# Performance work log

Hardware: AMD Instinct MI355X
Metric: run time of the kernel (lower is better)

The kernel has to match this reference:

```python
import jax, jax.numpy as jnp
import numpy as np

N, E, B = 100000, 1600000, 1024
EPS = 1e-5


def setup_inputs() -> dict:
    key = jax.random.key(0)
    ks = jax.random.split(key, 32)
    w = lambda k, shape: (jax.random.normal(k, shape, jnp.float32) * 0.05)
    inp = {
        'x': jax.random.normal(ks[0], (N, 20), jnp.float32),
        'edge_index': jax.random.randint(ks[1], (2, E), 0, N, dtype=jnp.int32),
        'batch': jnp.sort(jax.random.randint(ks[2], (N,), 0, B, dtype=jnp.int32)),
        # GCN layer 1 (20->64) + BN
        'W1': w(ks[3], (20, 64)), 'b1': jnp.zeros(64), 'g1': jnp.ones(64), 'bt1': jnp.zeros(64),
        # GCN layer 2 (64->64) + BN
        'W2': w(ks[4], (64, 64)), 'b2': jnp.zeros(64), 'g2': jnp.ones(64), 'bt2': jnp.zeros(64),
        # GCN layer 3 (64->128)
        'W3': w(ks[5], (64, 128)), 'b3': jnp.zeros(128),
        # operation head
        'Wo1': w(ks[6], (128, 64)), 'bo1': jnp.zeros(64), 'Wo2': w(ks[7], (64, 13)), 'bo2': jnp.zeros(13),
        # param head
        'Wp1': w(ks[8], (128, 64)), 'bp1': jnp.zeros(64), 'Wp2': w(ks[9], (64, 64)), 'bp2': jnp.zeros(64), 'Wp3': w(ks[10], (64, 1)), 'bp3': jnp.zeros(1),
        # done head
        'Wd1': w(ks[11], (128, 64)), 'bd1': jnp.zeros(64), 'Wd2': w(ks[12], (64, 2)), 'bd2': jnp.zeros(2),
    }
    return inp


def _gcn(x, W, b, src, dst):
    # PyG GCNConv: sym-normalized A+I, linear first, bias after aggregation
    h = x @ W  # [N, F]
    deg = jax.ops.segment_sum(jnp.ones_like(src, jnp.float32), dst, N) + 1.0  # +1 self loop
    dinv = jax.lax.rsqrt(deg)
    norm = dinv[src] * dinv[dst]  # [E]
    agg = jax.ops.segment_sum(h[src] * norm[:, None], dst, N)
    agg = agg + h * (dinv * dinv)[:, None]  # self-loop term
    return agg + b


def _bn(x, g, bt):
    mu = jnp.mean(x, axis=0)
    var = jnp.mean((x - mu) ** 2, axis=0)  # biased var (torch BN training math)
    return (x - mu) * jax.lax.rsqrt(var + EPS) * g + bt


def reference(x, edge_index, batch, W1, b1, g1, bt1, W2, b2, g2, bt2, W3, b3,
              Wo1, bo1, Wo2, bo2, Wp1, bp1, Wp2, bp2, Wp3, bp3, Wd1, bd1, Wd2, bd2):
    src, dst = edge_index[0], edge_index[1]
    h = jax.nn.relu(_bn(_gcn(x, W1, b1, src, dst), g1, bt1))  # dropout = identity (eval)
    h = jax.nn.relu(_bn(_gcn(h, W2, b2, src, dst), g2, bt2))
    h = _gcn(h, W3, b3, src, dst)  # [N, 128]
    # global mean pool over graphs
    sums = jax.ops.segment_sum(h, batch, B)
    cnt = jax.ops.segment_sum(jnp.ones((N,), jnp.float32), batch, B)
    enc = sums / jnp.maximum(cnt, 1.0)[:, None]  # [B, 128]
    op_logits = jax.nn.relu(enc @ Wo1 + bo1) @ Wo2 + bo2  # [B, 13]
    p = jax.nn.relu(enc @ Wp1 + bp1)
    p = jax.nn.relu(p @ Wp2 + bp2)
    param_value = p @ Wp3 + bp3  # [B, 1]
    done_logits = jax.nn.relu(enc @ Wd1 + bd1) @ Wd2 + bd2  # [B, 2]
    return op_logits, param_value, done_logits, enc
```

## Files before the change

kernel.cpp:

```cpp
#include <hip/hip_runtime.h>

#define BN_EPS 1e-5f

constexpr int BSH = 9;
constexpr int MAXB = 200;
constexpr int CAP = 12288;
constexpr int BINCAP = 32;
constexpr int FLUSH = 16;
constexpr int SBLK = 256;


__global__ void initk(int* __restrict__ gcur, float* __restrict__ bn, int NB) {
  int t = blockIdx.x * blockDim.x + threadIdx.x;
  if (t < NB) gcur[t] = t * CAP;
  if (t < 512) bn[t] = 0.f;
}

__global__ void bound_kernel(const int* __restrict__ batch, int* __restrict__ goffs, int N, int B) {
  int i = blockIdx.x * blockDim.x + threadIdx.x;
  if (i < N) {
    int b = batch[i];
    int p = (i == 0) ? -1 : batch[i - 1];
    for (int g = p + 1; g <= b; ++g) goffs[g] = i;
    if (i == N - 1) {
      for (int g = b + 1; g <= B; ++g) goffs[g] = N;
    }
  }
}


__global__ __launch_bounds__(256) void passA(const int* __restrict__ dst, const int* __restrict__ src,
                                             int* __restrict__ gcur, unsigned long long* __restrict__ temp,
                                             int E, int NB) {
  __shared__ unsigned long long bins[MAXB * BINCAP];
  __shared__ int bcnt[MAXB];
  int tid = threadIdx.x;
  for (int b = tid; b < NB; b += 256) bcnt[b] = 0;
  __syncthreads();
  int chunk = (E + gridDim.x - 1) / gridDim.x;
  int e0 = blockIdx.x * chunk;
  int e1 = min(e0 + chunk, E);
  for (int base = e0; base < e1; base += 1024) {
#pragma unroll
    for (int j = 0; j < 4; ++j) {
      int e = base + tid * 4 + j;
      if (e < e1) {
        int d = dst[e];
        int s = src[e];
        int b = d >> BSH;
        unsigned long long pk = ((unsigned long long)(unsigned)s << 32) | (unsigned)d;
        int slot = atomicAdd(&bcnt[b], 1);
        if (slot < BINCAP) {
          bins[b * BINCAP + slot] = pk;
        } else {
          int p = atomicAdd(&gcur[b], 1);
          temp[p] = pk;
        }
      }
    }
    __syncthreads();
    if (tid < NB) {
      int c = min(bcnt[tid], BINCAP);
      while (c >= FLUSH) {
        int p = atomicAdd(&gcur[tid], FLUSH);
        for (int j = 0; j < FLUSH; ++j) temp[p + j] = bins[tid * BINCAP + j];
        c -= FLUSH;
        for (int j = 0; j < c; ++j) bins[tid * BINCAP + j] = bins[tid * BINCAP + FLUSH + j];
      }
      bcnt[tid] = c;
    }
    __syncthreads();
  }
  if (tid < NB) {
    int c = min(bcnt[tid], BINCAP);
    if (c > 0) {
      int p = atomicAdd(&gcur[tid], c);
      for (int j = 0; j < c; ++j) temp[p + j] = bins[tid * BINCAP + j];
    }
  }
}

__global__ __launch_bounds__(512) void passB1(const unsigned long long* __restrict__ temp,
                                              const int* __restrict__ gcur,
                                              int* __restrict__ deg, float* __restrict__ dinv, int N) {
  __shared__ int h[512];
  int b = blockIdx.x, t = threadIdx.x;
  h[t] = 0;
  __syncthreads();
  int cnt = min(gcur[b] - b * CAP, CAP);
  const unsigned long long* tp = temp + (size_t)b * CAP;
  for (int i = t; i < cnt; i += 512) {
    int d = (int)(tp[i] & 0xffffffffu);
    atomicAdd(&h[d & 511], 1);
  }
  __syncthreads();
  int node = (b << BSH) + t;
  if (node < N) {
    deg[node] = h[t];
    dinv[node] = rsqrtf((float)h[t] + 1.f);
  }
}

__global__ __launch_bounds__(512) void passB2(const unsigned long long* __restrict__ temp,
                                              const int* __restrict__ gcur,
                                              const int* __restrict__ offs,
                                              int* __restrict__ csr, int N) {
  __shared__ int lofs[512];
  __shared__ int lcnt[512];
  int b = blockIdx.x, t = threadIdx.x;
  int node = (b << BSH) + t;
  lofs[t] = offs[min(node, N)];
  lcnt[t] = 0;
  __syncthreads();
  int cnt = min(gcur[b] - b * CAP, CAP);
  const unsigned long long* tp = temp + (size_t)b * CAP;
  for (int i = t; i < cnt; i += 512) {
    unsigned long long pk = tp[i];
    int d = (int)(pk & 0xffffffffu) & 511;
    int s = (int)(pk >> 32);
    int pos = lofs[d] + atomicAdd(&lcnt[d], 1);
    csr[pos] = s;
  }
}


__global__ __launch_bounds__(1024) void scan_p1(const int* __restrict__ cnt,
                                                int* __restrict__ offs,
                                                int* __restrict__ bsum, int n) {
  __shared__ int sh[1024];
  int t = threadIdx.x;
  int i = blockIdx.x * 1024 + t;
  int v = (i < n) ? cnt[i] : 0;
  sh[t] = v;
  __syncthreads();
  for (int d = 1; d < 1024; d <<= 1) {
    int x = (t >= d) ? sh[t - d] : 0;
    __syncthreads();
    sh[t] += x;
    __syncthreads();
  }
  if (i < n) offs[i] = sh[t] - v;
  if (t == 1023) bsum[blockIdx.x] = sh[t];
}

__global__ void scan_p2(int* __restrict__ bsum, int nb) {
  __shared__ int sh[128];
  int t = threadIdx.x;
  int v = (t < nb) ? bsum[t] : 0;
  sh[t] = v;
  __syncthreads();
  for (int d = 1; d < 128; d <<= 1) {
    int x = (t >= d) ? sh[t - d] : 0;
    __syncthreads();
    sh[t] += x;
    __syncthreads();
  }
  if (t < nb) bsum[t] = sh[t] - v;
}

__global__ __launch_bounds__(1024) void scan_p3(int* __restrict__ offs,
                                                const int* __restrict__ bsum, int n, int E) {
  int i = blockIdx.x * 1024 + threadIdx.x;
  if (i < n) offs[i] += bsum[blockIdx.x];
  if (i == 0) offs[n] = E;
}


__global__ __launch_bounds__(256) void agg32x_kernel(const float* __restrict__ x,
                                                     const int* __restrict__ offs,
                                                     const int* __restrict__ csr,
                                                     const float* __restrict__ dinv,
                                                     float* __restrict__ out, int n) {
  int lane = threadIdx.x & 63;
  int wid = threadIdx.x >> 6;
  int half = lane >> 5, f = lane & 31;
  bool act = f < 20;
  int gw = blockIdx.x * 4 + wid, nw = gridDim.x * 4;
  for (int i = gw; i < n; i += nw) {
    float acc = 0.f;
    if (!half && act) acc = x[(size_t)i * 20 + f] * dinv[i];
    int st = offs[i], en = offs[i + 1];
    for (int base = st; base < en; base += 64) {
      int idx = base + lane;
      int v = (idx < en) ? csr[idx] : 0;
      int cnt = min(64, en - base);
      int j = 0;
      for (; j + 3 < cnt; j += 4) {
        int s0 = __shfl(v, j + half);
        int s1 = __shfl(v, j + 2 + half);
        if (act) acc += x[(size_t)s0 * 20 + f] * dinv[s0] + x[(size_t)s1 * 20 + f] * dinv[s1];
      }
      for (; j < cnt; ++j) {
        int s = __shfl(v, j);
        if (!half && act) acc += x[(size_t)s * 20 + f] * dinv[s];
      }
    }
    acc += __shfl_xor(acc, 32);
    if (!half) out[(size_t)i * 32 + f] = acc;
  }
}

template <bool SCALE>
__global__ __launch_bounds__(256) void agg64t_kernel(const float* __restrict__ z,
                                                     const float* __restrict__ tav,
                                                     const float* __restrict__ tcv,
                                                     const int* __restrict__ offs,
                                                     const int* __restrict__ csr,
                                                     const float* __restrict__ dinv,
                                                     float* __restrict__ out, int n) {
  int lane = threadIdx.x & 63;
  int wid = threadIdx.x >> 6;
  float ta = tav[lane], tc = tcv[lane];
  int gw = blockIdx.x * 4 + wid, nw = gridDim.x * 4;
  for (int i = gw; i < n; i += nw) {
    float di = dinv[i];
    float acc = fmaxf(z[(size_t)i * 64 + lane] * ta + tc, 0.f) * di;
    int st = offs[i], en = offs[i + 1];
    for (int base = st; base < en; base += 64) {
      int idx = base + lane;
      int v = (idx < en) ? csr[idx] : 0;
      int cnt = min(64, en - base);
      int j = 0;
      for (; j + 3 < cnt; j += 4) {
        int s0 = __shfl(v, j), s1 = __shfl(v, j + 1);
        int s2 = __shfl(v, j + 2), s3 = __shfl(v, j + 3);
        float d0 = dinv[s0], d1 = dinv[s1], d2 = dinv[s2], d3 = dinv[s3];
        acc += fmaxf(z[(size_t)s0 * 64 + lane] * ta + tc, 0.f) * d0 +
               fmaxf(z[(size_t)s1 * 64 + lane] * ta + tc, 0.f) * d1 +
               fmaxf(z[(size_t)s2 * 64 + lane] * ta + tc, 0.f) * d2 +
               fmaxf(z[(size_t)s3 * 64 + lane] * ta + tc, 0.f) * d3;
      }
      for (; j < cnt; ++j) {
        int s = __shfl(v, j);
        acc += fmaxf(z[(size_t)s * 64 + lane] * ta + tc, 0.f) * dinv[s];
      }
    }
    if (SCALE) acc *= di;
    out[(size_t)i * 64 + lane] = acc;
  }
}


template <int K, int AS>
__global__ __launch_bounds__(256) void gemm_agg(const float* __restrict__ A, const float* __restrict__ W,
                                                const float* __restrict__ bias, const float* __restrict__ dinv,
                                                float* __restrict__ z, int n) {
  __shared__ float Ws[K * 64];
  __shared__ float As[128 * (K + 1)];
  int tid = threadIdx.x;
  int row0 = blockIdx.x * 128;
  for (int i = tid; i < K * 64; i += 256) Ws[i] = W[i];
  for (int i = tid; i < 128 * K; i += 256) {
    int r = i / K, k = i - r * K;
    int gr = row0 + r;
    As[r * (K + 1) + k] = (gr < n) ? A[(size_t)gr * AS + k] : 0.f;
  }
  __syncthreads();
  int rg = tid >> 2;
  int fs = tid & 3;
  float acc0[16], acc1[16];
#pragma unroll
  for (int j = 0; j < 16; ++j) { acc0[j] = 0.f; acc1[j] = 0.f; }
  const float* a0 = &As[(2 * rg) * (K + 1)];
  const float* a1 = &As[(2 * rg + 1) * (K + 1)];
  const float* wb = &Ws[fs * 16];
  for (int k = 0; k < K; ++k) {
    float x0 = a0[k], x1 = a1[k];
#pragma unroll
    for (int j = 0; j < 16; ++j) {
      float w = wb[k * 64 + j];
      acc0[j] += x0 * w;
      acc1[j] += x1 * w;
    }
  }
  int r0 = row0 + 2 * rg;
  if (r0 < n) {
    float dv = dinv[r0];
    float4* zp = (float4*)&z[(size_t)r0 * 64 + fs * 16];
#pragma unroll
    for (int j = 0; j < 16; j += 4)
      zp[j >> 2] = make_float4(acc0[j] * dv + bias[fs * 16 + j], acc0[j + 1] * dv + bias[fs * 16 + j + 1],
                               acc0[j + 2] * dv + bias[fs * 16 + j + 2], acc0[j + 3] * dv + bias[fs * 16 + j + 3]);
  }
  int r1 = r0 + 1;
  if (r1 < n) {
    float dv = dinv[r1];
    float4* zp = (float4*)&z[(size_t)r1 * 64 + fs * 16];
#pragma unroll
    for (int j = 0; j < 16; j += 4)
      zp[j >> 2] = make_float4(acc1[j] * dv + bias[fs * 16 + j], acc1[j + 1] * dv + bias[fs * 16 + j + 1],
                               acc1[j + 2] * dv + bias[fs * 16 + j + 2], acc1[j + 3] * dv + bias[fs * 16 + j + 3]);
  }
}


__global__ __launch_bounds__(256) void bn_stats(const float* __restrict__ z,
                                                float* __restrict__ partial, int N) {
  int lane = threadIdx.x & 63, wid = threadIdx.x >> 6;
  int gw = blockIdx.x * 4 + wid, nw = gridDim.x * 4;
  float s = 0.f, q = 0.f;
  for (int r = gw; r < N; r += nw) {
    float v = z[(size_t)r * 64 + lane];
    s += v;
    q += v * v;
  }
  __shared__ float sh[2][4][64];
  sh[0][wid][lane] = s;
  sh[1][wid][lane] = q;
  __syncthreads();
  if (wid == 0) {
    float ts = sh[0][0][lane] + sh[0][1][lane] + sh[0][2][lane] + sh[0][3][lane];
    float tq = sh[1][0][lane] + sh[1][1][lane] + sh[1][2][lane] + sh[1][3][lane];
    partial[blockIdx.x * 128 + lane] = ts;
    partial[blockIdx.x * 128 + 64 + lane] = tq;
  }
}

__global__ __launch_bounds__(1024) void bn_final_kernel(const float* __restrict__ partial,
                                                        const float* __restrict__ g,
                                                        const float* __restrict__ bt,
                                                        float* __restrict__ a, float* __restrict__ c,
                                                        float n) {
  __shared__ float sh[16][128];
  int t = threadIdx.x;
  int grp = t >> 6, lane = t & 63;
  float s = 0.f, q = 0.f;
#pragma unroll
  for (int k = 0; k < 16; ++k) {
    int i = grp * 16 + k;
    s += partial[i * 128 + lane];
    q += partial[i * 128 + 64 + lane];
  }
  sh[grp][lane] = s;
  sh[grp][64 + lane] = q;
  __syncthreads();
  for (int str = 8; str >= 1; str >>= 1) {
    if (grp < str) {
      sh[grp][lane] += sh[grp + str][lane];
      sh[grp][64 + lane] += sh[grp + str][64 + lane];
    }
    __syncthreads();
  }
  if (grp == 0) {
    float mu = sh[0][lane] / n;
    float var = fmaxf(sh[0][64 + lane] / n - mu * mu, 0.f);
    float rstd = rsqrtf(var + BN_EPS);
    float av = g[lane] * rstd;
    a[lane] = av;
    c[lane] = bt[lane] - mu * av;
  }
}


__global__ __launch_bounds__(64) void pool_kernel(const float* __restrict__ v3,
                                                  const int* __restrict__ goffs,
                                                  float* __restrict__ ep, int B) {
  int b = blockIdx.x, t = threadIdx.x;
  int st = goffs[b], en = goffs[b + 1];
  float s = 0.f;
  int r = st;
  for (; r + 1 < en; r += 2) s += v3[(size_t)r * 64 + t] + v3[(size_t)(r + 1) * 64 + t];
  if (r < en) s += v3[(size_t)r * 64 + t];
  int c = en - st;
  ep[(size_t)b * 64 + t] = s / (float)max(c, 1);
}


__global__ __launch_bounds__(256) void heads_kernel(
    const float* __restrict__ ep, const int* __restrict__ goffs,
    const float* __restrict__ W3, const float* __restrict__ b3,
    const float* __restrict__ Wo1, const float* __restrict__ bo1,
    const float* __restrict__ Wo2, const float* __restrict__ bo2,
    const float* __restrict__ Wp1, const float* __restrict__ bp1,
    const float* __restrict__ Wp2, const float* __restrict__ bp2,
    const float* __restrict__ Wp3, const float* __restrict__ bp3,
    const float* __restrict__ Wd1, const float* __restrict__ bd1,
    const float* __restrict__ Wd2, const float* __restrict__ bd2,
    float* __restrict__ out_op, float* __restrict__ out_p, float* __restrict__ out_d,
    float* __restrict__ enc_out, int B) {
  __shared__ float epl[16 * 64];
  __shared__ float es[16 * 128];
  __shared__ float t1[16 * 64];
  __shared__ float t2[16 * 64];
  int tid = threadIdx.x;
  int g0 = blockIdx.x * 16;
  for (int i = tid; i < 16 * 64; i += 256) epl[i] = ep[(size_t)g0 * 64 + i];
  __syncthreads();
  for (int o = tid; o < 16 * 128; o += 256) {
    int r = o >> 7, c = o & 127;
    float a = b3[c];
    for (int k = 0; k < 64; ++k) a += epl[r * 64 + k] * W3[k * 128 + c];
    if (goffs[g0 + r + 1] - goffs[g0 + r] == 0) a = 0.f;
    es[o] = a;
    enc_out[(size_t)(g0 + r) * 128 + c] = a;
  }
  __syncthreads();
  for (int o = tid; o < 16 * 64; o += 256) {
    int r = o >> 6, c = o & 63;
    float a = bo1[c];
    for (int k = 0; k < 128; k++) a += es[r * 128 + k] * Wo1[k * 64 + c];
    t1[o] = fmaxf(a, 0.f);
  }
  __syncthreads();
  for (int o = tid; o < 16 * 13; o += 256) {
    int r = o / 13, c = o - r * 13;
    float a = bo2[c];
    for (int k = 0; k < 64; k++) a += t1[r * 64 + k] * Wo2[k * 13 + c];
    out_op[(size_t)(g0 + r) * 13 + c] = a;
  }
  __syncthreads();
  for (int o = tid; o < 16 * 64; o += 256) {
    int r = o >> 6, c = o & 63;
    float a = bp1[c];
    for (int k = 0; k < 128; k++) a += es[r * 128 + k] * Wp1[k * 64 + c];
    t1[o] = fmaxf(a, 0.f);
  }
  __syncthreads();
  for (int o = tid; o < 16 * 64; o += 256) {
    int r = o >> 6, c = o & 63;
    float a = bp2[c];
    for (int k = 0; k < 64; k++) a += t1[r * 64 + k] * Wp2[k * 64 + c];
    t2[o] = fmaxf(a, 0.f);
  }
  __syncthreads();
  for (int o = tid; o < 16; o += 256) {
    float a = bp3[0];
    for (int k = 0; k < 64; k++) a += t2[o * 64 + k] * Wp3[k];
    out_p[g0 + o] = a;
  }
  __syncthreads();
  for (int o = tid; o < 16 * 64; o += 256) {
    int r = o >> 6, c = o & 63;
    float a = bd1[c];
    for (int k = 0; k < 128; k++) a += es[r * 128 + k] * Wd1[k * 64 + c];
    t1[o] = fmaxf(a, 0.f);
  }
  __syncthreads();
  for (int o = tid; o < 16 * 2; o += 256) {
    int r = o >> 1, c = o & 1;
    float a = bd2[c];
    for (int k = 0; k < 64; k++) a += t1[r * 64 + k] * Wd2[k * 2 + c];
    out_d[(size_t)(g0 + r) * 2 + c] = a;
  }
}


extern "C" void kernel_launch(void* const* d_in, const int* in_sizes, int n_in,
                              void* d_out, int out_size, void* d_ws, size_t ws_size,
                              hipStream_t stream) {
  const float* x   = (const float*)d_in[0];
  const int*   ei  = (const int*)d_in[1];
  const int*   bat = (const int*)d_in[2];
  const float* W1 = (const float*)d_in[3];  const float* b1  = (const float*)d_in[4];
  const float* g1 = (const float*)d_in[5];  const float* bt1 = (const float*)d_in[6];
  const float* W2 = (const float*)d_in[7];  const float* b2  = (const float*)d_in[8];
  const float* g2 = (const float*)d_in[9];  const float* bt2 = (const float*)d_in[10];
  const float* W3 = (const float*)d_in[11]; const float* b3  = (const float*)d_in[12];
  const float* Wo1 = (const float*)d_in[13]; const float* bo1 = (const float*)d_in[14];
  const float* Wo2 = (const float*)d_in[15]; const float* bo2 = (const float*)d_in[16];
  const float* Wp1 = (const float*)d_in[17]; const float* bp1 = (const float*)d_in[18];
  const float* Wp2 = (const float*)d_in[19]; const float* bp2 = (const float*)d_in[20];
  const float* Wp3 = (const float*)d_in[21]; const float* bp3 = (const float*)d_in[22];
  const float* Wd1 = (const float*)d_in[23]; const float* bd1 = (const float*)d_in[24];
  const float* Wd2 = (const float*)d_in[25]; const float* bd2 = (const float*)d_in[26];

  int N = in_sizes[0] / 20;
  int E = in_sizes[1] / 2;
  int B = out_size / 144;
  const int* esrc = ei;
  const int* edst = ei + E;
  int NB = (N + (1 << BSH) - 1) >> BSH;

  char* ws = (char*)d_ws;
  size_t off = 0;
  auto alloc = [&](size_t bytes) -> char* {
    char* p = ws + off;
    off = (off + bytes + 255) & ~(size_t)255;
    return p;
  };
  int*   gcur  = (int*)alloc((size_t)NB * 4);
  int*   deg   = (int*)alloc((size_t)N * 4);
  float* dinv  = (float*)alloc((size_t)N * 4);
  int*   offs  = (int*)alloc(((size_t)N + 1) * 4);
  int*   bsum  = (int*)alloc(128 * 4);
  int*   goffs = (int*)alloc(((size_t)B + 1) * 4);
  float* bn    = (float*)alloc(512 * 4);
  float* partial = (float*)alloc((size_t)SBLK * 128 * 4);
  unsigned long long* temp = (unsigned long long*)alloc((size_t)NB * CAP * 8);
  int*   csr   = (int*)alloc((size_t)E * 4);
  float* bufA  = (float*)alloc((size_t)N * 64 * 4);
  float* bufB  = (float*)alloc((size_t)N * 64 * 4);
  float* ep    = (float*)alloc((size_t)B * 64 * 4);

  float* ta1 = bn + 256, *tc1 = bn + 320;
  float* ta2 = bn + 384, *tc2 = bn + 448;

  float* out_op = (float*)d_out;
  float* out_p  = out_op + (size_t)B * 13;
  float* out_d  = out_p + B;
  float* enc    = out_d + (size_t)B * 2;

  hipLaunchKernelGGL(initk, dim3(2), dim3(256), 0, stream, gcur, bn, NB);
  hipLaunchKernelGGL(bound_kernel, dim3((N + 255) / 256), dim3(256), 0, stream, bat, goffs, N, B);
  hipLaunchKernelGGL(passA, dim3(256), dim3(256), 0, stream, edst, esrc, gcur, temp, E, NB);
  hipLaunchKernelGGL(passB1, dim3(NB), dim3(512), 0, stream, temp, gcur, deg, dinv, N);
  int nb1 = (N + 1023) / 1024;
  hipLaunchKernelGGL(scan_p1, dim3(nb1), dim3(1024), 0, stream, deg, offs, bsum, N);
  hipLaunchKernelGGL(scan_p2, dim3(1), dim3(128), 0, stream, bsum, nb1);
  hipLaunchKernelGGL(scan_p3, dim3(nb1), dim3(1024), 0, stream, offs, bsum, N, E);
  hipLaunchKernelGGL(passB2, dim3(NB), dim3(512), 0, stream, temp, gcur, offs, csr, N);

  int gblocks = (N + 127) / 128;
  hipLaunchKernelGGL(agg32x_kernel, dim3(2048), dim3(256), 0, stream, x, offs, csr, dinv, bufA, N);
  hipLaunchKernelGGL((gemm_agg<20, 32>), dim3(gblocks), dim3(256), 0, stream,
                     bufA, W1, b1, dinv, bufB, N);
  hipLaunchKernelGGL(bn_stats, dim3(SBLK), dim3(256), 0, stream, bufB, partial, N);
  hipLaunchKernelGGL(bn_final_kernel, dim3(1), dim3(1024), 0, stream,
                     partial, g1, bt1, ta1, tc1, (float)N);
  hipLaunchKernelGGL((agg64t_kernel<false>), dim3(2048), dim3(256), 0, stream,
                     bufB, ta1, tc1, offs, csr, dinv, bufA, N);
  hipLaunchKernelGGL((gemm_agg<64, 64>), dim3(gblocks), dim3(256), 0, stream,
                     bufA, W2, b2, dinv, bufB, N);
  hipLaunchKernelGGL(bn_stats, dim3(SBLK), dim3(256), 0, stream, bufB, partial, N);
  hipLaunchKernelGGL(bn_final_kernel, dim3(1), dim3(1024), 0, stream,
                     partial, g2, bt2, ta2, tc2, (float)N);
  hipLaunchKernelGGL((agg64t_kernel<true>), dim3(2048), dim3(256), 0, stream,
                     bufB, ta2, tc2, offs, csr, dinv, bufA, N);
  hipLaunchKernelGGL(pool_kernel, dim3(B), dim3(64), 0, stream, bufA, goffs, ep, B);
  hipLaunchKernelGGL(heads_kernel, dim3(B / 16), dim3(256), 0, stream, ep, goffs, W3, b3,
                     Wo1, bo1, Wo2, bo2, Wp1, bp1, Wp2, bp2, Wp3, bp3, Wd1, bd1, Wd2, bd2,
                     out_op, out_p, out_d, enc, B);
}
```

Measured before the change: 532.8 us.

## Store gathered node features in bf16 to halve gather traffic

The per-node feature tables read by the edge-gather kernels (the input x pre-scaled by dinv, and the GEMM outputs z) are now stored as bf16 with round-to-nearest-even packing. A new prex kernel pre-multiplies x by dinv and pads each row to 32 columns, which removes the per-edge dinv load and the inactive-lane branch in the first aggregation. The aim is to cut the bytes moved by the random-access gathers, which dominate the runtime. In exchange there is an extra kernel launch and reduced precision in the intermediate activations and in the BN statistics.

```diff
diff --git a/kernel.cpp b/kernel.cpp
--- a/kernel.cpp
+++ b/kernel.cpp
@@ -8,6 +8,17 @@
 constexpr int BINCAP = 32;
 constexpr int FLUSH = 16;
 constexpr int SBLK = 256;
+
+typedef unsigned short u16;
+typedef unsigned int u32;
+
+__device__ __forceinline__ float b2f(u16 h) {
+  return __uint_as_float(((u32)h) << 16);
+}
+__device__ __forceinline__ u16 f2b(float f) {
+  u32 u = __float_as_uint(f);
+  return (u16)((u + 0x7FFFu + ((u >> 16) & 1u)) >> 16);
+}
 
 
 __global__ void initk(int* __restrict__ gcur, float* __restrict__ bn, int NB) {
@@ -166,19 +177,27 @@
 }
 
 
-__global__ __launch_bounds__(256) void agg32x_kernel(const float* __restrict__ x,
+__global__ void prex_kernel(const float* __restrict__ x, const float* __restrict__ dinv,
+                            u16* __restrict__ x16, int N) {
+  int stride = gridDim.x * blockDim.x;
+  for (int i = blockIdx.x * blockDim.x + threadIdx.x; i < N * 32; i += stride) {
+    int row = i >> 5, f = i & 31;
+    float v = (f < 20) ? x[row * 20 + f] * dinv[row] : 0.f;
+    x16[i] = f2b(v);
+  }
+}
+
+
+__global__ __launch_bounds__(256) void agg32x_kernel(const u16* __restrict__ x16,
                                                      const int* __restrict__ offs,
                                                      const int* __restrict__ csr,
-                                                     const float* __restrict__ dinv,
                                                      float* __restrict__ out, int n) {
   int lane = threadIdx.x & 63;
   int wid = threadIdx.x >> 6;
   int half = lane >> 5, f = lane & 31;
-  bool act = f < 20;
   int gw = blockIdx.x * 4 + wid, nw = gridDim.x * 4;
   for (int i = gw; i < n; i += nw) {
-    float acc = 0.f;
-    if (!half && act) acc = x[(size_t)i * 20 + f] * dinv[i];
+    float acc = half ? 0.f : b2f(x16[(size_t)i * 32 + f]);
     int st = offs[i], en = offs[i + 1];
     for (int base = st; base < en; base += 64) {
       int idx = base + lane;
@@ -188,11 +207,11 @@
       for (; j + 3 < cnt; j += 4) {
         int s0 = __shfl(v, j + half);
         int s1 = __shfl(v, j + 2 + half);
-        if (act) acc += x[(size_t)s0 * 20 + f] * dinv[s0] + x[(size_t)s1 * 20 + f] * dinv[s1];
+        acc += b2f(x16[(size_t)s0 * 32 + f]) + b2f(x16[(size_t)s1 * 32 + f]);
       }
       for (; j < cnt; ++j) {
         int s = __shfl(v, j);
-        if (!half && act) acc += x[(size_t)s * 20 + f] * dinv[s];
+        if (!half) acc += b2f(x16[(size_t)s * 32 + f]);
       }
     }
     acc += __shfl_xor(acc, 32);
@@ -201,7 +220,7 @@
 }
 
 template <bool SCALE>
-__global__ __launch_bounds__(256) void agg64t_kernel(const float* __restrict__ z,
+__global__ __launch_bounds__(256) void agg64t_kernel(const u16* __restrict__ z16,
                                                      const float* __restrict__ tav,
                                                      const float* __restrict__ tcv,
                                                      const int* __restrict__ offs,
@@ -214,7 +233,7 @@
   int gw = blockIdx.x * 4 + wid, nw = gridDim.x * 4;
   for (int i = gw; i < n; i += nw) {
     float di = dinv[i];
-    float acc = fmaxf(z[(size_t)i * 64 + lane] * ta + tc, 0.f) * di;
+    float acc = fmaxf(b2f(z16[(size_t)i * 64 + lane]) * ta + tc, 0.f) * di;
     int st = offs[i], en = offs[i + 1];
     for (int base = st; base < en; base += 64) {
       int idx = base + lane;
@@ -225,14 +244,14 @@
         int s0 = __shfl(v, j), s1 = __shfl(v, j + 1);
         int s2 = __shfl(v, j + 2), s3 = __shfl(v, j + 3);
         float d0 = dinv[s0], d1 = dinv[s1], d2 = dinv[s2], d3 = dinv[s3];
-        acc += fmaxf(z[(size_t)s0 * 64 + lane] * ta + tc, 0.f) * d0 +
-               fmaxf(z[(size_t)s1 * 64 + lane] * ta + tc, 0.f) * d1 +
-               fmaxf(z[(size_t)s2 * 64 + lane] * ta + tc, 0.f) * d2 +
-               fmaxf(z[(size_t)s3 * 64 + lane] * ta + tc, 0.f) * d3;
+        acc += fmaxf(b2f(z16[(size_t)s0 * 64 + lane]) * ta + tc, 0.f) * d0 +
+               fmaxf(b2f(z16[(size_t)s1 * 64 + lane]) * ta + tc, 0.f) * d1 +
+               fmaxf(b2f(z16[(size_t)s2 * 64 + lane]) * ta + tc, 0.f) * d2 +
+               fmaxf(b2f(z16[(size_t)s3 * 64 + lane]) * ta + tc, 0.f) * d3;
       }
       for (; j < cnt; ++j) {
         int s = __shfl(v, j);
-        acc += fmaxf(z[(size_t)s * 64 + lane] * ta + tc, 0.f) * dinv[s];
+        acc += fmaxf(b2f(z16[(size_t)s * 64 + lane]) * ta + tc, 0.f) * dinv[s];
       }
     }
     if (SCALE) acc *= di;
@@ -244,7 +263,7 @@
 template <int K, int AS>
 __global__ __launch_bounds__(256) void gemm_agg(const float* __restrict__ A, const float* __restrict__ W,
                                                 const float* __restrict__ bias, const float* __restrict__ dinv,
-                                                float* __restrict__ z, int n) {
+                                                u16* __restrict__ z16, int n) {
   __shared__ float Ws[K * 64];
   __shared__ float As[128 * (K + 1)];
   int tid = threadIdx.x;
@@ -273,34 +292,45 @@
       acc1[j] += x1 * w;
     }
   }
+  int base = fs * 16;
   int r0 = row0 + 2 * rg;
   if (r0 < n) {
     float dv = dinv[r0];
-    float4* zp = (float4*)&z[(size_t)r0 * 64 + fs * 16];
+    u32 pk[8];
 #pragma unroll
-    for (int j = 0; j < 16; j += 4)
-      zp[j >> 2] = make_float4(acc0[j] * dv + bias[fs * 16 + j], acc0[j + 1] * dv + bias[fs * 16 + j + 1],
-                               acc0[j + 2] * dv + bias[fs * 16 + j + 2], acc0[j + 3] * dv + bias[fs * 16 + j + 3]);
+    for (int j = 0; j < 8; ++j) {
+      float o0 = acc0[2 * j] * dv + bias[base + 2 * j];
+      float o1 = acc0[2 * j + 1] * dv + bias[base + 2 * j + 1];
+      pk[j] = (u32)f2b(o0) | ((u32)f2b(o1) << 16);
+    }
+    uint4* zp = (uint4*)&z16[(size_t)r0 * 64 + base];
+    zp[0] = make_uint4(pk[0], pk[1], pk[2], pk[3]);
+    zp[1] = make_uint4(pk[4], pk[5], pk[6], pk[7]);
   }
   int r1 = r0 + 1;
   if (r1 < n) {
     float dv = dinv[r1];
-    float4* zp = (float4*)&z[(size_t)r1 * 64 + fs * 16];
+    u32 pk[8];
 #pragma unroll
-    for (int j = 0; j < 16; j += 4)
-      zp[j >> 2] = make_float4(acc1[j] * dv + bias[fs * 16 + j], acc1[j + 1] * dv + bias[fs * 16 + j + 1],
-                               acc1[j + 2] * dv + bias[fs * 16 + j + 2], acc1[j + 3] * dv + bias[fs * 16 + j + 3]);
-  }
-}
-
-
-__global__ __launch_bounds__(256) void bn_stats(const float* __restrict__ z,
+    for (int j = 0; j < 8; ++j) {
+      float o0 = acc1[2 * j] * dv + bias[base + 2 * j];
+      float o1 = acc1[2 * j + 1] * dv + bias[base + 2 * j + 1];
+      pk[j] = (u32)f2b(o0) | ((u32)f2b(o1) << 16);
+    }
+    uint4* zp = (uint4*)&z16[(size_t)r1 * 64 + base];
+    zp[0] = make_uint4(pk[0], pk[1], pk[2], pk[3]);
+    zp[1] = make_uint4(pk[4], pk[5], pk[6], pk[7]);
+  }
+}
+
+
+__global__ __launch_bounds__(256) void bn_stats(const u16* __restrict__ z16,
                                                 float* __restrict__ partial, int N) {
   int lane = threadIdx.x & 63, wid = threadIdx.x >> 6;
   int gw = blockIdx.x * 4 + wid, nw = gridDim.x * 4;
   float s = 0.f, q = 0.f;
   for (int r = gw; r < N; r += nw) {
-    float v = z[(size_t)r * 64 + lane];
+    float v = b2f(z16[(size_t)r * 64 + lane]);
     s += v;
     q += v * v;
   }
@@ -488,8 +518,9 @@
   float* partial = (float*)alloc((size_t)SBLK * 128 * 4);
   unsigned long long* temp = (unsigned long long*)alloc((size_t)NB * CAP * 8);
   int*   csr   = (int*)alloc((size_t)E * 4);
-  float* bufA  = (float*)alloc((size_t)N * 64 * 4);
-  float* bufB  = (float*)alloc((size_t)N * 64 * 4);
+  u16*   x16   = (u16*)alloc((size_t)N * 32 * 2);
+  u16*   z16   = (u16*)alloc((size_t)N * 64 * 2);
+  float* aggf  = (float*)alloc((size_t)N * 64 * 4);
   float* ep    = (float*)alloc((size_t)B * 64 * 4);
 
   float* ta1 = bn + 256, *tc1 = bn + 320;
@@ -511,22 +542,23 @@
   hipLaunchKernelGGL(passB2, dim3(NB), dim3(512), 0, stream, temp, gcur, offs, csr, N);
 
   int gblocks = (N + 127) / 128;
-  hipLaunchKernelGGL(agg32x_kernel, dim3(2048), dim3(256), 0, stream, x, offs, csr, dinv, bufA, N);
+  hipLaunchKernelGGL(prex_kernel, dim3(2048), dim3(256), 0, stream, x, dinv, x16, N);
+  hipLaunchKernelGGL(agg32x_kernel, dim3(2048), dim3(256), 0, stream, x16, offs, csr, aggf, N);
   hipLaunchKernelGGL((gemm_agg<20, 32>), dim3(gblocks), dim3(256), 0, stream,
-                     bufA, W1, b1, dinv, bufB, N);
-  hipLaunchKernelGGL(bn_stats, dim3(SBLK), dim3(256), 0, stream, bufB, partial, N);
+                     aggf, W1, b1, dinv, z16, N);
+  hipLaunchKernelGGL(bn_stats, dim3(SBLK), dim3(256), 0, stream, z16, partial, N);
   hipLaunchKernelGGL(bn_final_kernel, dim3(1), dim3(1024), 0, stream,
                      partial, g1, bt1, ta1, tc1, (float)N);
   hipLaunchKernelGGL((agg64t_kernel<false>), dim3(2048), dim3(256), 0, stream,
-                     bufB, ta1, tc1, offs, csr, dinv, bufA, N);
+                     z16, ta1, tc1, offs, csr, dinv, aggf, N);
   hipLaunchKernelGGL((gemm_agg<64, 64>), dim3(gblocks), dim3(256), 0, stream,
-                     bufA, W2, b2, dinv, bufB, N);
-  hipLaunchKernelGGL(bn_stats, dim3(SBLK), dim3(256), 0, stream, bufB, partial, N);
+                     aggf, W2, b2, dinv, z16, N);
+  hipLaunchKernelGGL(bn_stats, dim3(SBLK), dim3(256), 0, stream, z16, partial, N);
   hipLaunchKernelGGL(bn_final_kernel, dim3(1), dim3(1024), 0, stream,
                      partial, g2, bt2, ta2, tc2, (float)N);
   hipLaunchKernelGGL((agg64t_kernel<true>), dim3(2048), dim3(256), 0, stream,
-                     bufB, ta2, tc2, offs, csr, dinv, bufA, N);
-  hipLaunchKernelGGL(pool_kernel, dim3(B), dim3(64), 0, stream, bufA, goffs, ep, B);
+                     z16, ta2, tc2, offs, csr, dinv, aggf, N);
+  hipLaunchKernelGGL(pool_kernel, dim3(B), dim3(64), 0, stream, aggf, goffs, ep, B);
   hipLaunchKernelGGL(heads_kernel, dim3(B / 16), dim3(256), 0, stream, ep, goffs, W3, b3,
                      Wo1, bo1, Wo2, bo2, Wp1, bp1, Wp2, bp2, Wp3, bp3, Wd1, bd1, Wd2, bd2,
                      out_op, out_p, out_d, enc, B);
```

Measured after the change: 496.6 us. 1.07x faster.
